# Performance work log

Hardware: AMD Instinct MI355X
Metric: run time of the kernel (lower is better)

Reference implementation:

```python
import jax, jax.numpy as jnp
import numpy as np

N_NODES = 100000
N_EDGES = 1600000
IN_FEAT = 256
OUT_FEAT = 128


def setup_inputs() -> dict:
    key = jax.random.key(0)
    ks = jax.random.split(key, 8)
    x = jax.random.normal(ks[0], (N_NODES, IN_FEAT), dtype=jnp.float32)
    rows0 = jnp.sort(jax.random.randint(ks[1], (N_EDGES,), 0, N_NODES, dtype=jnp.int32))
    cols0 = jax.random.randint(ks[2], (N_EDGES,), 0, N_NODES, dtype=jnp.int32)
    vals0 = jax.random.uniform(ks[3], (N_EDGES,), dtype=jnp.float32)
    rows1 = jnp.sort(jax.random.randint(ks[4], (N_EDGES,), 0, N_NODES, dtype=jnp.int32))
    cols1 = jax.random.randint(ks[5], (N_EDGES,), 0, N_NODES, dtype=jnp.int32)
    vals1 = jax.random.uniform(ks[6], (N_EDGES,), dtype=jnp.float32)
    kw0, kw1 = jax.random.split(ks[7])
    # glorot-uniform-ish scale for [IN_FEAT, OUT_FEAT]
    limit = float(np.sqrt(6.0 / (IN_FEAT + OUT_FEAT)))
    W0 = jax.random.uniform(kw0, (IN_FEAT, OUT_FEAT), minval=-limit, maxval=limit, dtype=jnp.float32)
    W1 = jax.random.uniform(kw1, (IN_FEAT, OUT_FEAT), minval=-limit, maxval=limit, dtype=jnp.float32)
    return {"x": x, "rows0": rows0, "cols0": cols0, "vals0": vals0,
            "rows1": rows1, "cols1": cols1, "vals1": vals1, "W0": W0, "W1": W1}


def _spmm(rows, cols, vals, dense, n_rows):
    # sparse [N,N] (COO) @ dense [N,D] -> [N,D]
    gathered = vals[:, None] * dense[cols]          # [E, D]
    return jax.ops.segment_sum(gathered, rows, num_segments=n_rows)


def reference(x, rows0, cols0, vals0, rows1, cols1, vals1, W0, W1):
    # GraphConvolution with dropout=0 (identity), featureless=False, no bias, relu.
    # support_i = A_i @ (x @ W_i); output = relu(sum_i support_i)
    s0 = _spmm(rows0, cols0, vals0, x @ W0, N_NODES)
    s1 = _spmm(rows1, cols1, vals1, x @ W1, N_NODES)
    return jax.nn.relu(s0 + s1)
```

## Files before the change

kernel.cpp:

```cpp
#include <hip/hip_runtime.h>
#include <hip/hip_bf16.h>
#include <stdint.h>

#define NN   100000
#define NE   1600000
#define KIN  256
#define FOUT 128

typedef __attribute__((ext_vector_type(8))) short short8;
typedef __attribute__((ext_vector_type(4))) float f32x4;
typedef __attribute__((ext_vector_type(2))) float f32x2;

static __device__ __forceinline__ unsigned short f2bf(float f) {
  unsigned int u = __float_as_uint(f);
  u += 0x7fffu + ((u >> 16) & 1u);
  return (unsigned short)(u >> 16);
}

static __device__ __forceinline__ short8 pack8(float4 u, float4 v) {
  short8 r;
  r[0] = (short)f2bf(u.x); r[1] = (short)f2bf(u.y);
  r[2] = (short)f2bf(u.z); r[3] = (short)f2bf(u.w);
  r[4] = (short)f2bf(v.x); r[5] = (short)f2bf(v.y);
  r[6] = (short)f2bf(v.z); r[7] = (short)f2bf(v.w);
  return r;
}

__global__ void convert_w(const float* __restrict__ W0, const float* __restrict__ W1,
                          unsigned short* __restrict__ wt) {
  int n = blockIdx.x;
  int k = threadIdx.x;
  int which = blockIdx.y;
  const float* W = which ? W1 : W0;
  wt[(size_t)which * (FOUT * KIN) + n * KIN + k] = f2bf(W[k * FOUT + n]);
}

__global__ __launch_bounds__(256) void build_rowptr(const int* __restrict__ rows0,
                                                    const int* __restrict__ rows1,
                                                    int* __restrict__ rp0,
                                                    int* __restrict__ rp1) {
  const int e = blockIdx.x * 256 + threadIdx.x;
  const int* rows = blockIdx.y ? rows1 : rows0;
  int* rp = blockIdx.y ? rp1 : rp0;
  int r1 = rows[e];
  int r2 = (e + 1 < NE) ? rows[e + 1] : NN;
  if (e == 0)
    for (int r = 0; r <= r1; ++r) rp[r] = 0;
  for (int r = r1 + 1; r <= r2; ++r) rp[r] = e + 1;
}

__global__ __launch_bounds__(512, 4) void gemm_fused(const float* __restrict__ x,
                                                     const unsigned short* __restrict__ wt,
                                                     unsigned short* __restrict__ h) {
  __shared__ __align__(16) unsigned short bbuf[2][2 * 128 * 64];

  const int tid  = threadIdx.x;
  const int lane = tid & 63;
  const int wv   = tid >> 6;
  const int m    = lane & 15;
  const int quad = lane >> 4;
  const int rowbase = blockIdx.x * 128 + wv * 16;

  int r  = rowbase + m;
  int rc = r < NN ? r : NN - 1;
  const float* ap = x + (size_t)rc * KIN + quad * 8;

  f32x4 acc[2][8];
#pragma unroll
  for (int t = 0; t < 2; ++t)
#pragma unroll
    for (int n = 0; n < 8; ++n)
      acc[t][n] = (f32x4){0.f, 0.f, 0.f, 0.f};

#define STAGE_DMA(ko_, buf_) do {                                              \
    _Pragma("unroll")                                                          \
    for (int u = 0; u < 4; ++u) {                                              \
      int pid = u * 512 + tid;                                                 \
      int tm = pid >> 10; int c = (pid >> 3) & 127; int s = pid & 7;           \
      const unsigned short* g = wt + (size_t)tm * (FOUT * KIN) + c * KIN +     \
                                (ko_) + ((s ^ (c & 7)) * 8);                   \
      __builtin_amdgcn_global_load_lds(                                        \
          (const __attribute__((address_space(1))) void*)g,                    \
          (__attribute__((address_space(3))) void*)                            \
              &bbuf[buf_][(size_t)(u * 512 + wv * 64) * 8],                    \
          16, 0, 0);                                                           \
    } } while (0)

  float4 fc0 = *(const float4*)(ap);
  float4 fc1 = *(const float4*)(ap + 4);

  STAGE_DMA(0, 0);
  __syncthreads();

#pragma unroll
  for (int ci = 0; ci < 4; ++ci) {
    if (ci < 3) STAGE_DMA((ci + 1) * 64, (ci + 1) & 1);
#pragma unroll
    for (int kk = 0; kk < 2; ++kk) {
      const int ki = ci * 2 + kk;
      float4 fn0, fn1;
      if (ki < 7) {
        fn0 = *(const float4*)(ap + (ki + 1) * 32);
        fn1 = *(const float4*)(ap + (ki + 1) * 32 + 4);
      }
      short8 a = pack8(fc0, fc1);
      const unsigned short* bb = &bbuf[ci & 1][0];
#pragma unroll
      for (int t = 0; t < 2; ++t)
#pragma unroll
        for (int n = 0; n < 8; ++n) {
          const int col = n * 16 + m;
          short8 b = *(const short8*)(bb + t * 8192 + col * 64 +
                                      (((kk * 4 + quad) ^ (m & 7)) * 8));
          acc[t][n] = __builtin_amdgcn_mfma_f32_16x16x32_bf16(a, b, acc[t][n], 0, 0, 0);
        }
      fc0 = fn0; fc1 = fn1;
    }
    if (ci < 3) __syncthreads();
  }
#undef STAGE_DMA

  unsigned short* tile = &bbuf[0][0] + wv * 2048;
#pragma unroll
  for (int t = 0; t < 2; ++t) {
#pragma unroll
    for (int n = 0; n < 8; ++n)
#pragma unroll
      for (int reg = 0; reg < 4; ++reg)
        tile[(quad * 4 + reg) * 128 + n * 16 + m] = f2bf(acc[t][n][reg]);

    unsigned short* hh = h + (size_t)t * NN * FOUT;
#pragma unroll
    for (int p = 0; p < 4; ++p) {
      int row = p * 4 + quad;
      uint4 v = *(const uint4*)&tile[row * 128 + m * 8];
      int grow = rowbase + row;
      if (grow < NN)
        *(uint4*)&hh[(size_t)grow * FOUT + m * 8] = v;
    }
  }
}

static __device__ __forceinline__ void consume8(const float* __restrict__ vals, int i,
                                                const unsigned* g, float& sx, float& sy) {
#pragma unroll
  for (int u = 0; u < 8; ++u) {
    float v = vals[i + u];
    sx += v * __uint_as_float(g[u] << 16);
    sy += v * __uint_as_float(g[u] & 0xffff0000u);
  }
}

static __device__ __forceinline__ void tail_spmm(const int* __restrict__ cols,
                                                 const float* __restrict__ vals,
                                                 const unsigned short* __restrict__ hsrc,
                                                 int i, int e, int fo,
                                                 float& sx, float& sy) {
  for (; i + 4 <= e; i += 4) {
    int c0 = cols[i], c1 = cols[i + 1], c2 = cols[i + 2], c3 = cols[i + 3];
    unsigned g0 = *(const unsigned*)(hsrc + (size_t)c0 * FOUT + fo);
    unsigned g1 = *(const unsigned*)(hsrc + (size_t)c1 * FOUT + fo);
    unsigned g2 = *(const unsigned*)(hsrc + (size_t)c2 * FOUT + fo);
    unsigned g3 = *(const unsigned*)(hsrc + (size_t)c3 * FOUT + fo);
    float v0 = vals[i], v1 = vals[i + 1], v2 = vals[i + 2], v3 = vals[i + 3];
    sx += v0 * __uint_as_float(g0 << 16);
    sy += v0 * __uint_as_float(g0 & 0xffff0000u);
    sx += v1 * __uint_as_float(g1 << 16);
    sy += v1 * __uint_as_float(g1 & 0xffff0000u);
    sx += v2 * __uint_as_float(g2 << 16);
    sy += v2 * __uint_as_float(g2 & 0xffff0000u);
    sx += v3 * __uint_as_float(g3 << 16);
    sy += v3 * __uint_as_float(g3 & 0xffff0000u);
  }
  for (; i < e; ++i) {
    int c = cols[i];
    float v = vals[i];
    unsigned g = *(const unsigned*)(hsrc + (size_t)c * FOUT + fo);
    sx += v * __uint_as_float(g << 16);
    sy += v * __uint_as_float(g & 0xffff0000u);
  }
}

__global__ __launch_bounds__(256) void spmm_relu(
    const int* __restrict__ rp0, const int* __restrict__ cols0, const float* __restrict__ vals0,
    const int* __restrict__ rp1, const int* __restrict__ cols1, const float* __restrict__ vals1,
    const unsigned short* __restrict__ h, float* __restrict__ out) {
  const int lane = threadIdx.x & 63;
  int r = blockIdx.x * 4 + (threadIdx.x >> 6);
  r = __builtin_amdgcn_readfirstlane(r);
  const int fo = lane * 2;

  const unsigned short* h0 = h;
  const unsigned short* h1 = h + (size_t)NN * FOUT;

  int i0 = __builtin_amdgcn_readfirstlane(rp0[r]);
  int e0 = __builtin_amdgcn_readfirstlane(rp0[r + 1]);
  int i1 = __builtin_amdgcn_readfirstlane(rp1[r]);
  int e1 = __builtin_amdgcn_readfirstlane(rp1[r + 1]);

  float sx = 0.f, sy = 0.f;

  while (i0 + 8 <= e0 && i1 + 8 <= e1) {
    unsigned g0[8], g1[8];
#pragma unroll
    for (int u = 0; u < 8; ++u) {
      int c = cols0[i0 + u];
      g0[u] = *(const unsigned*)(h0 + (size_t)c * FOUT + fo);
    }
#pragma unroll
    for (int u = 0; u < 8; ++u) {
      int c = cols1[i1 + u];
      g1[u] = *(const unsigned*)(h1 + (size_t)c * FOUT + fo);
    }
    consume8(vals0, i0, g0, sx, sy);
    consume8(vals1, i1, g1, sx, sy);
    i0 += 8;
    i1 += 8;
  }
  tail_spmm(cols0, vals0, h0, i0, e0, fo, sx, sy);
  tail_spmm(cols1, vals1, h1, i1, e1, fo, sx, sy);

  f32x2 o;
  o.x = sx > 0.f ? sx : 0.f;
  o.y = sy > 0.f ? sy : 0.f;
  __builtin_nontemporal_store(o, (f32x2*)(out + (size_t)r * FOUT + fo));
}

extern "C" void kernel_launch(void* const* d_in, const int* in_sizes, int n_in,
                              void* d_out, int out_size, void* d_ws, size_t ws_size,
                              hipStream_t stream) {
  const float* x     = (const float*)d_in[0];
  const int*   rows0 = (const int*)d_in[1];
  const int*   cols0 = (const int*)d_in[2];
  const float* vals0 = (const float*)d_in[3];
  const int*   rows1 = (const int*)d_in[4];
  const int*   cols1 = (const int*)d_in[5];
  const float* vals1 = (const float*)d_in[6];
  const float* W0    = (const float*)d_in[7];
  const float* W1    = (const float*)d_in[8];
  float* out = (float*)d_out;

  char* ws = (char*)d_ws;
  unsigned short* wt = (unsigned short*)(ws);
  unsigned short* h  = (unsigned short*)(ws + 131072);
  int* rp0 = (int*)(ws + 51331072);
  int* rp1 = (int*)(ws + 51731136);

  build_rowptr<<<dim3(6250, 2), 256, 0, stream>>>(rows0, rows1, rp0, rp1);
  convert_w<<<dim3(128, 2), 256, 0, stream>>>(W0, W1, wt);
  gemm_fused<<<dim3((NN + 127) / 128, 1), 512, 0, stream>>>(x, wt, h);
  spmm_relu<<<25000, 256, 0, stream>>>(rp0, cols0, vals0, rp1, cols1, vals1, h, out);
}
```

Before: 332.2 us.

## Stage full bf16 weights in LDS once and merge prep kernels into one launch

The GEMM kernel now loads the entire bf16 weight matrix for both layers (128 KB) into shared memory at once, replacing the double-buffered K-chunk pipeline and its intermediate barriers. It also loads all of a row's x activations up front rather than prefetching them chunk by chunk. The rowptr build and weight conversion kernels are merged into a single launch to cut one launch's overhead. The larger LDS footprint lowers occupancy (launch bounds drop from 4 to 2 blocks), and the weight load and the compute no longer overlap.

Result: slower. 345.1 us (+3.9%).

```diff
diff --git a/kernel.cpp b/kernel.cpp
--- a/kernel.cpp
+++ b/kernel.cpp
@@ -26,33 +26,40 @@
   return r;
 }
 
-__global__ void convert_w(const float* __restrict__ W0, const float* __restrict__ W1,
-                          unsigned short* __restrict__ wt) {
-  int n = blockIdx.x;
-  int k = threadIdx.x;
-  int which = blockIdx.y;
-  const float* W = which ? W1 : W0;
-  wt[(size_t)which * (FOUT * KIN) + n * KIN + k] = f2bf(W[k * FOUT + n]);
-}
-
-__global__ __launch_bounds__(256) void build_rowptr(const int* __restrict__ rows0,
-                                                    const int* __restrict__ rows1,
-                                                    int* __restrict__ rp0,
-                                                    int* __restrict__ rp1) {
-  const int e = blockIdx.x * 256 + threadIdx.x;
-  const int* rows = blockIdx.y ? rows1 : rows0;
-  int* rp = blockIdx.y ? rp1 : rp0;
-  int r1 = rows[e];
-  int r2 = (e + 1 < NE) ? rows[e + 1] : NN;
-  if (e == 0)
-    for (int r = 0; r <= r1; ++r) rp[r] = 0;
-  for (int r = r1 + 1; r <= r2; ++r) rp[r] = e + 1;
-}
-
-__global__ __launch_bounds__(512, 4) void gemm_fused(const float* __restrict__ x,
+__global__ __launch_bounds__(256) void prep(const int* __restrict__ rows0,
+                                            const int* __restrict__ rows1,
+                                            int* __restrict__ rp0,
+                                            int* __restrict__ rp1,
+                                            const float* __restrict__ W0,
+                                            const float* __restrict__ W1,
+                                            unsigned short* __restrict__ wt) {
+  const int b = blockIdx.x;
+  if (b < 12500) {
+    const int sub = b >= 6250 ? b - 6250 : b;
+    const int mat = b >= 6250;
+    const int e = sub * 256 + threadIdx.x;
+    const int* rows = mat ? rows1 : rows0;
+    int* rp = mat ? rp1 : rp0;
+    int r1 = rows[e];
+    int r2 = (e + 1 < NE) ? rows[e + 1] : NN;
+    if (e == 0)
+      for (int r = 0; r <= r1; ++r) rp[r] = 0;
+    for (int r = r1 + 1; r <= r2; ++r) rp[r] = e + 1;
+  } else {
+    const int idx = (b - 12500) * 256 + threadIdx.x;
+    const int which = idx >> 15;
+    const int rem = idx & 0x7fff;
+    const int n = rem >> 8;
+    const int k = rem & 255;
+    const float* W = which ? W1 : W0;
+    wt[(size_t)which * (FOUT * KIN) + n * KIN + k] = f2bf(W[k * FOUT + n]);
+  }
+}
+
+__global__ __launch_bounds__(512, 2) void gemm_fused(const float* __restrict__ x,
                                                      const unsigned short* __restrict__ wt,
                                                      unsigned short* __restrict__ h) {
-  __shared__ __align__(16) unsigned short bbuf[2][2 * 128 * 64];
+  __shared__ __align__(16) unsigned short bbuf[2 * 128 * 256];
 
   const int tid  = threadIdx.x;
   const int lane = tid & 63;
@@ -65,6 +72,19 @@
   int rc = r < NN ? r : NN - 1;
   const float* ap = x + (size_t)rc * KIN + quad * 8;
 
+#pragma unroll
+  for (int u = 0; u < 16; ++u) {
+    int pid = u * 512 + tid;
+    int tm = pid >> 12; int c = (pid >> 5) & 127; int s = pid & 31;
+    const unsigned short* g = wt + (size_t)tm * (FOUT * KIN) + c * KIN +
+                              ((s ^ (c & 7)) * 8);
+    __builtin_amdgcn_global_load_lds(
+        (const __attribute__((address_space(1))) void*)g,
+        (__attribute__((address_space(3))) void*)
+            &bbuf[(size_t)(u * 512 + wv * 64) * 8],
+        16, 0, 0);
+  }
+
   f32x4 acc[2][8];
 #pragma unroll
   for (int t = 0; t < 2; ++t)
@@ -72,55 +92,32 @@
     for (int n = 0; n < 8; ++n)
       acc[t][n] = (f32x4){0.f, 0.f, 0.f, 0.f};
 
-#define STAGE_DMA(ko_, buf_) do {                                              \
-    _Pragma("unroll")                                                          \
-    for (int u = 0; u < 4; ++u) {                                              \
-      int pid = u * 512 + tid;                                                 \
-      int tm = pid >> 10; int c = (pid >> 3) & 127; int s = pid & 7;           \
-      const unsigned short* g = wt + (size_t)tm * (FOUT * KIN) + c * KIN +     \
-                                (ko_) + ((s ^ (c & 7)) * 8);                   \
-      __builtin_amdgcn_global_load_lds(                                        \
-          (const __attribute__((address_space(1))) void*)g,                    \
-          (__attribute__((address_space(3))) void*)                            \
-              &bbuf[buf_][(size_t)(u * 512 + wv * 64) * 8],                    \
-          16, 0, 0);                                                           \
-    } } while (0)
-
-  float4 fc0 = *(const float4*)(ap);
-  float4 fc1 = *(const float4*)(ap + 4);
-
-  STAGE_DMA(0, 0);
   __syncthreads();
 
-#pragma unroll
-  for (int ci = 0; ci < 4; ++ci) {
-    if (ci < 3) STAGE_DMA((ci + 1) * 64, (ci + 1) & 1);
-#pragma unroll
-    for (int kk = 0; kk < 2; ++kk) {
-      const int ki = ci * 2 + kk;
-      float4 fn0, fn1;
-      if (ki < 7) {
-        fn0 = *(const float4*)(ap + (ki + 1) * 32);
-        fn1 = *(const float4*)(ap + (ki + 1) * 32 + 4);
+  float4 f[16];
+#pragma unroll
+  for (int s = 0; s < 8; ++s) {
+    f[2 * s]     = *(const float4*)(ap + s * 32);
+    f[2 * s + 1] = *(const float4*)(ap + s * 32 + 4);
+  }
+
+#pragma unroll
+  for (int s = 0; s < 8; ++s) {
+    short8 a = pack8(f[2 * s], f[2 * s + 1]);
+#pragma unroll
+    for (int t = 0; t < 2; ++t)
+#pragma unroll
+      for (int n = 0; n < 8; ++n) {
+        const int col = n * 16 + m;
+        short8 b = *(const short8*)(&bbuf[0] + t * 32768 + col * 256 +
+                                    (((s * 4 + quad) ^ (m & 7)) * 8));
+        acc[t][n] = __builtin_amdgcn_mfma_f32_16x16x32_bf16(a, b, acc[t][n], 0, 0, 0);
       }
-      short8 a = pack8(fc0, fc1);
-      const unsigned short* bb = &bbuf[ci & 1][0];
-#pragma unroll
-      for (int t = 0; t < 2; ++t)
-#pragma unroll
-        for (int n = 0; n < 8; ++n) {
-          const int col = n * 16 + m;
-          short8 b = *(const short8*)(bb + t * 8192 + col * 64 +
-                                      (((kk * 4 + quad) ^ (m & 7)) * 8));
-          acc[t][n] = __builtin_amdgcn_mfma_f32_16x16x32_bf16(a, b, acc[t][n], 0, 0, 0);
-        }
-      fc0 = fn0; fc1 = fn1;
-    }
-    if (ci < 3) __syncthreads();
-  }
-#undef STAGE_DMA
-
-  unsigned short* tile = &bbuf[0][0] + wv * 2048;
+  }
+
+  __syncthreads();
+
+  unsigned short* tile = &bbuf[0] + wv * 2048;
 #pragma unroll
   for (int t = 0; t < 2; ++t) {
 #pragma unroll
@@ -246,8 +243,7 @@
   int* rp0 = (int*)(ws + 51331072);
   int* rp1 = (int*)(ws + 51731136);
 
-  build_rowptr<<<dim3(6250, 2), 256, 0, stream>>>(rows0, rows1, rp0, rp1);
-  convert_w<<<dim3(128, 2), 256, 0, stream>>>(W0, W1, wt);
+  prep<<<12756, 256, 0, stream>>>(rows0, rows1, rp0, rp1, W0, W1, wt);
   gemm_fused<<<dim3((NN + 127) / 128, 1), 512, 0, stream>>>(x, wt, h);
   spmm_relu<<<25000, 256, 0, stream>>>(rp0, cols0, vals0, rp1, cols1, vals1, h, out);
 }
```
